# Kernel tuning notes

Measured on AMD Instinct MI355X. Metric: run time of the kernel, lower is better.

## Reference

```python
import jax, jax.numpy as jnp
import numpy as np

B, M, D, DH, DV = 16384, 3, 2048, 1024, 512

def setup_inputs() -> dict:
    key = jax.random.key(0)
    kx, kq, kk, kv, kf = jax.random.split(key, 5)
    x = jax.random.normal(kx, (B, M, D), dtype=jnp.float32)
    # nn.Linear weights are [out, in]; q/k/v scaled by 1/32 as in __init__
    Wq = jax.random.normal(kq, (DH, D), dtype=jnp.float32) / 32.0
    Wk = jax.random.normal(kk, (DH, D), dtype=jnp.float32) / 32.0
    Wv = jax.random.normal(kv, (DV, D), dtype=jnp.float32) / 32.0
    Wfc = jax.random.normal(kf, (1, DV), dtype=jnp.float32)
    return {"x": x, "Wq": Wq, "Wk": Wk, "Wv": Wv, "Wfc": Wfc}

def reference(x, Wq, Wk, Wv, Wfc):
    # q,k: [B,M,DH]; v: [B,M,DV]
    q = jnp.einsum('bmd,hd->bmh', x, Wq)
    k = jnp.einsum('bmd,hd->bmh', x, Wk)
    v = jnp.einsum('bmd,vd->bmv', x, Wv)
    qk = jnp.einsum('bih,bjh->bij', q, k)          # [B,M,M]
    attn = jax.nn.softmax(qk, axis=2)
    attn = jnp.sum(attn, axis=1) / M               # [B,M] (sum over queries, avg)
    z = jnp.einsum('bm,bmv->bv', attn, v)          # [B,DV]
    return z @ Wfc.T                               # [B,1]
```

## Files before the change

### kernel.cpp

```cpp
#include <hip/hip_runtime.h>
#include <hip/hip_bf16.h>
#include <stdint.h>
#include <stddef.h>

#define B_   16384
#define M_   3
#define D_   2048
#define DH_  1024
#define DV_  512
#define ROWS (B_ * M_)
#define NOUT (2 * DH_)

typedef _Float16 f16;
typedef f16   f16x8 __attribute__((ext_vector_type(8)));
typedef float f32x4 __attribute__((ext_vector_type(4)));

__device__ __forceinline__ void async16(const void* g, void* l) {
  __builtin_amdgcn_global_load_lds(
      (const __attribute__((address_space(1))) void*)g,
      (__attribute__((address_space(3))) void*)l, 16, 0, 0);
}

__global__ void k_wvf(const float* __restrict__ Wv, const float* __restrict__ Wfc,
                      float* __restrict__ wvf) {
  int dl = threadIdx.x & 31;
  int vs = threadIdx.x >> 5;
  int d = blockIdx.x * 32 + dl;
  float acc = 0.f;
  #pragma unroll 8
  for (int v = vs * 64; v < vs * 64 + 64; ++v)
    acc += Wfc[v] * Wv[(size_t)v * D_ + d];
  __shared__ float red[8][32];
  red[vs][dl] = acc;
  __syncthreads();
  if (threadIdx.x < 32) {
    float s = 0.f;
    #pragma unroll
    for (int i = 0; i < 8; ++i) s += red[i][threadIdx.x];
    wvf[blockIdx.x * 32 + threadIdx.x] = s;
  }
}

__global__ void k_castw(const float* __restrict__ Wq, const float* __restrict__ Wk,
                        f16* __restrict__ Wh) {
  int t = blockIdx.x * 256 + threadIdx.x;
  int idx = t * 8;
  int j = idx >> 11;
  int d = idx & (D_ - 1);
  const float* src = (j < DH_) ? (Wq + (size_t)j * D_ + d)
                               : (Wk + (size_t)(j - DH_) * D_ + d);
  f32x4 a = *(const f32x4*)src;
  f32x4 b = *(const f32x4*)(src + 4);
  f16x8 h;
  h[0] = (f16)a[0]; h[1] = (f16)a[1]; h[2] = (f16)a[2]; h[3] = (f16)a[3];
  h[4] = (f16)b[0]; h[5] = (f16)b[1]; h[6] = (f16)b[2]; h[7] = (f16)b[3];
  *(f16x8*)(Wh + (size_t)idx) = h;
}

__global__ void k_prep(const float* __restrict__ x, const float* __restrict__ wvf,
                       f16* __restrict__ Xh, float* __restrict__ vf) {
  int w = threadIdx.x >> 6, lane = threadIdx.x & 63;
  int row = blockIdx.x * 4 + w;
  const float* xr = x + (size_t)row * D_;
  f16* xo = Xh + (size_t)row * D_;
  float acc = 0.f;
  #pragma unroll
  for (int p = 0; p < 4; ++p) {
    int col = p * 512 + lane * 8;
    f32x4 a = *(const f32x4*)(xr + col);
    f32x4 b = *(const f32x4*)(xr + col + 4);
    f32x4 wa = *(const f32x4*)(wvf + col);
    f32x4 wb = *(const f32x4*)(wvf + col + 4);
    f16x8 h;
    h[0] = (f16)a[0]; h[1] = (f16)a[1]; h[2] = (f16)a[2]; h[3] = (f16)a[3];
    h[4] = (f16)b[0]; h[5] = (f16)b[1]; h[6] = (f16)b[2]; h[7] = (f16)b[3];
    *(f16x8*)(xo + col) = h;
    acc += a[0]*wa[0] + a[1]*wa[1] + a[2]*wa[2] + a[3]*wa[3]
         + b[0]*wb[0] + b[1]*wb[1] + b[2]*wb[2] + b[3]*wb[3];
  }
  #pragma unroll
  for (int off = 1; off < 64; off <<= 1) acc += __shfl_xor(acc, off);
  if (lane == 0) vf[row] = acc;
}

__global__ __launch_bounds__(256, 3) void k_gemm(const f16* __restrict__ Xh,
                                                 const f16* __restrict__ Wh,
                                                 f16* __restrict__ QK) {
  const int ct = blockIdx.x;
  const int rt = blockIdx.y;
  const int tid = threadIdx.x;
  const int w = tid >> 6, lane = tid & 63;
  const int wr = w >> 1, wc = w & 1;

  __shared__ __align__(16) f16 lds_a[128 * 64];
  __shared__ __align__(16) f16 lds_b[128 * 64];

  f32x4 acc[4][4] = {};

  const int srow = lane >> 3;
  const int schunk = (lane & 7) ^ srow;
  const int scol = schunk * 8;

  const f16* gA[4]; const f16* gB[4];
  f16 *la[4], *lb[4];
  #pragma unroll
  for (int t = 0; t < 4; ++t) {
    int rowA = w * 32 + t * 8;
    gA[t] = Xh + (size_t)(rt * 128 + rowA + srow) * D_ + scol;
    gB[t] = Wh + (size_t)(ct * 128 + rowA + srow) * D_ + scol;
    la[t] = &lds_a[rowA * 64];
    lb[t] = &lds_b[rowA * 64];
  }

  const int m = lane & 15;
  const int kq = lane >> 4;
  const f16* fa0 = &lds_a[(size_t)(wr * 64 + m) * 64 + ((kq    ) ^ (m & 7)) * 8];
  const f16* fa1 = &lds_a[(size_t)(wr * 64 + m) * 64 + ((kq + 4) ^ (m & 7)) * 8];
  const f16* fb0 = &lds_b[(size_t)(wc * 64 + m) * 64 + ((kq    ) ^ (m & 7)) * 8];
  const f16* fb1 = &lds_b[(size_t)(wc * 64 + m) * 64 + ((kq + 4) ^ (m & 7)) * 8];

  for (int k0 = 0; k0 < D_; k0 += 64) {
    #pragma unroll
    for (int t = 0; t < 4; ++t) async16(gA[t] + k0, la[t]);
    #pragma unroll
    for (int t = 0; t < 4; ++t) async16(gB[t] + k0, lb[t]);
    __syncthreads();
    {
      f16x8 af[4], bf[4];
      #pragma unroll
      for (int i = 0; i < 4; ++i) af[i] = *(const f16x8*)(fa0 + i * 16 * 64);
      #pragma unroll
      for (int j = 0; j < 4; ++j) bf[j] = *(const f16x8*)(fb0 + j * 16 * 64);
      #pragma unroll
      for (int i = 0; i < 4; ++i)
        #pragma unroll
        for (int j = 0; j < 4; ++j)
          acc[i][j] = __builtin_amdgcn_mfma_f32_16x16x32_f16(af[i], bf[j], acc[i][j], 0, 0, 0);
    }
    {
      f16x8 af[4], bf[4];
      #pragma unroll
      for (int i = 0; i < 4; ++i) af[i] = *(const f16x8*)(fa1 + i * 16 * 64);
      #pragma unroll
      for (int j = 0; j < 4; ++j) bf[j] = *(const f16x8*)(fb1 + j * 16 * 64);
      #pragma unroll
      for (int i = 0; i < 4; ++i)
        #pragma unroll
        for (int j = 0; j < 4; ++j)
          acc[i][j] = __builtin_amdgcn_mfma_f32_16x16x32_f16(af[i], bf[j], acc[i][j], 0, 0, 0);
    }
    __syncthreads();
  }

  const int r0 = rt * 128 + wr * 64 + (lane >> 4) * 4;
  const int c0 = ct * 128 + wc * 64 + (lane & 15);
  #pragma unroll
  for (int i = 0; i < 4; ++i)
    #pragma unroll
    for (int j = 0; j < 4; ++j)
      #pragma unroll
      for (int r = 0; r < 4; ++r)
        QK[(size_t)(r0 + i * 16 + r) * NOUT + (c0 + j * 16)] = (f16)acc[i][j][r];
}

__global__ void k_attn(const f16* __restrict__ QK, const float* __restrict__ vf,
                       float* __restrict__ out) {
  int w = threadIdx.x >> 6, lane = threadIdx.x & 63;
  int b = blockIdx.x * 4 + w;
  const f16* base = QK + (size_t)b * M_ * NOUT;
  f16x8 q[3][2], k[3][2];
  #pragma unroll
  for (int i = 0; i < 3; ++i) {
    q[i][0] = *(const f16x8*)(base + i * NOUT + lane * 8);
    q[i][1] = *(const f16x8*)(base + i * NOUT + 512 + lane * 8);
    k[i][0] = *(const f16x8*)(base + i * NOUT + 1024 + lane * 8);
    k[i][1] = *(const f16x8*)(base + i * NOUT + 1536 + lane * 8);
  }
  float s[3][3];
  #pragma unroll
  for (int i = 0; i < 3; ++i)
    #pragma unroll
    for (int j = 0; j < 3; ++j) {
      float a = 0.f;
      #pragma unroll
      for (int c = 0; c < 2; ++c)
        #pragma unroll
        for (int t = 0; t < 8; ++t)
          a += (float)q[i][c][t] * (float)k[j][c][t];
      s[i][j] = a;
    }
  #pragma unroll
  for (int i = 0; i < 3; ++i)
    #pragma unroll
    for (int j = 0; j < 3; ++j)
      #pragma unroll
      for (int off = 1; off < 64; off <<= 1)
        s[i][j] += __shfl_xor(s[i][j], off);
  if (lane == 0) {
    float attn[3] = {0.f, 0.f, 0.f};
    #pragma unroll
    for (int i = 0; i < 3; ++i) {
      float m = fmaxf(s[i][0], fmaxf(s[i][1], s[i][2]));
      float e0 = expf(s[i][0] - m), e1 = expf(s[i][1] - m), e2 = expf(s[i][2] - m);
      float inv = 1.f / (e0 + e1 + e2);
      attn[0] += e0 * inv; attn[1] += e1 * inv; attn[2] += e2 * inv;
    }
    float o = attn[0] * vf[b * 3 + 0] + attn[1] * vf[b * 3 + 1] + attn[2] * vf[b * 3 + 2];
    out[b] = o * (1.f / 3.f);
  }
}

extern "C" void kernel_launch(void* const* d_in, const int* in_sizes, int n_in,
                              void* d_out, int out_size, void* d_ws, size_t ws_size,
                              hipStream_t stream) {
  const float* x   = (const float*)d_in[0];
  const float* Wq  = (const float*)d_in[1];
  const float* Wk  = (const float*)d_in[2];
  const float* Wv  = (const float*)d_in[3];
  const float* Wfc = (const float*)d_in[4];
  float* out = (float*)d_out;

  char* ws = (char*)d_ws;
  f16*   Xh  = (f16*)(ws);
  f16*   QK  = (f16*)(ws + 201326592ull);
  f16*   Wh  = (f16*)(ws + 402653184ull);
  float* wvf = (float*)(ws + 411041792ull);
  float* vf  = (float*)(ws + 411049984ull);

  k_wvf  <<<64,             256, 0, stream>>>(Wv, Wfc, wvf);
  k_castw<<<2048,           256, 0, stream>>>(Wq, Wk, Wh);
  k_prep <<<ROWS / 4,       256, 0, stream>>>(x, wvf, Xh, vf);
  k_gemm <<<dim3(16, 384),  256, 0, stream>>>(Xh, Wh, QK);
  k_attn <<<B_ / 4,         256, 0, stream>>>(QK, vf, out);
}
```

Before: 1.011 ms.

## Fuse QK dot products into GEMM epilogue with per-head-tile partial scores

The GEMM's column tiles now pair 64 Q columns with the matching 64 K columns, and row tiles are aligned to 42 whole batches of 126 rows. Each block stages its Q and K tile in LDS and computes partial 3x3 scores over its 64-head slice, writing 144 floats per batch instead of the full fp16 QK matrix. A small final kernel sums the partials and applies softmax. This removes the large QK write and read-back at the cost of roughly 2% wasted rows in the padded tiles and a serial LDS epilogue.

New measurement: 976.8 us. 1.03x faster.

```diff
diff --git a/kernel.cpp b/kernel.cpp
--- a/kernel.cpp
+++ b/kernel.cpp
@@ -9,7 +9,10 @@
 #define DH_  1024
 #define DV_  512
 #define ROWS (B_ * M_)
-#define NOUT (2 * DH_)
+#define RT_ROWS 126
+#define RT_BATCH 42
+#define NRT 391
+#define NHT 16
 
 typedef _Float16 f16;
 typedef f16   f16x8 __attribute__((ext_vector_type(8)));
@@ -85,8 +88,8 @@
 
 __global__ __launch_bounds__(256, 3) void k_gemm(const f16* __restrict__ Xh,
                                                  const f16* __restrict__ Wh,
-                                                 f16* __restrict__ QK) {
-  const int ct = blockIdx.x;
+                                                 float* __restrict__ S_part) {
+  const int ht = blockIdx.x;
   const int rt = blockIdx.y;
   const int tid = threadIdx.x;
   const int w = tid >> 6, lane = tid & 63;
@@ -105,11 +108,15 @@
   f16 *la[4], *lb[4];
   #pragma unroll
   for (int t = 0; t < 4; ++t) {
-    int rowA = w * 32 + t * 8;
-    gA[t] = Xh + (size_t)(rt * 128 + rowA + srow) * D_ + scol;
-    gB[t] = Wh + (size_t)(ct * 128 + rowA + srow) * D_ + scol;
-    la[t] = &lds_a[rowA * 64];
-    lb[t] = &lds_b[rowA * 64];
+    int rowT = w * 32 + t * 8;
+    int ra = rt * RT_ROWS + rowT + srow;
+    if (ra > ROWS - 1) ra = ROWS - 1;
+    gA[t] = Xh + (size_t)ra * D_ + scol;
+    int c = rowT + srow;
+    int rb = (c < 64) ? (ht * 64 + c) : (DH_ + ht * 64 + (c - 64));
+    gB[t] = Wh + (size_t)rb * D_ + scol;
+    la[t] = &lds_a[rowT * 64];
+    lb[t] = &lds_b[rowT * 64];
   }
 
   const int m = lane & 15;
@@ -152,62 +159,58 @@
     __syncthreads();
   }
 
-  const int r0 = rt * 128 + wr * 64 + (lane >> 4) * 4;
-  const int c0 = ct * 128 + wc * 64 + (lane & 15);
-  #pragma unroll
-  for (int i = 0; i < 4; ++i)
-    #pragma unroll
-    for (int j = 0; j < 4; ++j)
-      #pragma unroll
-      for (int r = 0; r < 4; ++r)
-        QK[(size_t)(r0 + i * 16 + r) * NOUT + (c0 + j * 16)] = (f16)acc[i][j][r];
-}
-
-__global__ void k_attn(const f16* __restrict__ QK, const float* __restrict__ vf,
-                       float* __restrict__ out) {
-  int w = threadIdx.x >> 6, lane = threadIdx.x & 63;
-  int b = blockIdx.x * 4 + w;
-  const f16* base = QK + (size_t)b * M_ * NOUT;
-  f16x8 q[3][2], k[3][2];
+  {
+    f16* dst = wc ? lds_b : lds_a;
+    const int rbase = wr * 64 + (lane >> 4) * 4;
+    const int hcol = lane & 15;
+    #pragma unroll
+    for (int i = 0; i < 4; ++i)
+      #pragma unroll
+      for (int j = 0; j < 4; ++j)
+        #pragma unroll
+        for (int r = 0; r < 4; ++r)
+          dst[(size_t)(rbase + i * 16 + r) * 64 + j * 16 + hcol] = (f16)acc[i][j][r];
+  }
+  __syncthreads();
+
+  for (int p = tid; p < RT_BATCH * 9; p += 256) {
+    int bl = p / 9;
+    int ij = p - bl * 9;
+    int i = ij / 3, j = ij - i * 3;
+    const f16* qp = &lds_a[(size_t)(bl * 3 + i) * 64];
+    const f16* kp = &lds_b[(size_t)(bl * 3 + j) * 64];
+    float s = 0.f;
+    #pragma unroll
+    for (int hc = 0; hc < 8; ++hc) {
+      f16x8 qa = *(const f16x8*)(qp + hc * 8);
+      f16x8 ka = *(const f16x8*)(kp + hc * 8);
+      #pragma unroll
+      for (int t = 0; t < 8; ++t) s += (float)qa[t] * (float)ka[t];
+    }
+    int b = rt * RT_BATCH + bl;
+    if (b < B_) S_part[(size_t)b * (NHT * 9) + ht * 9 + ij] = s;
+  }
+}
+
+__global__ void k_final(const float* __restrict__ S_part, const float* __restrict__ vf,
+                        float* __restrict__ out) {
+  int b = blockIdx.x * 256 + threadIdx.x;
+  const float* sp = S_part + (size_t)b * (NHT * 9);
+  float s[9] = {0,0,0,0,0,0,0,0,0};
+  #pragma unroll
+  for (int ht = 0; ht < NHT; ++ht)
+    #pragma unroll
+    for (int ij = 0; ij < 9; ++ij) s[ij] += sp[ht * 9 + ij];
+  float attn[3] = {0.f, 0.f, 0.f};
   #pragma unroll
   for (int i = 0; i < 3; ++i) {
-    q[i][0] = *(const f16x8*)(base + i * NOUT + lane * 8);
-    q[i][1] = *(const f16x8*)(base + i * NOUT + 512 + lane * 8);
-    k[i][0] = *(const f16x8*)(base + i * NOUT + 1024 + lane * 8);
-    k[i][1] = *(const f16x8*)(base + i * NOUT + 1536 + lane * 8);
-  }
-  float s[3][3];
-  #pragma unroll
-  for (int i = 0; i < 3; ++i)
-    #pragma unroll
-    for (int j = 0; j < 3; ++j) {
-      float a = 0.f;
-      #pragma unroll
-      for (int c = 0; c < 2; ++c)
-        #pragma unroll
-        for (int t = 0; t < 8; ++t)
-          a += (float)q[i][c][t] * (float)k[j][c][t];
-      s[i][j] = a;
-    }
-  #pragma unroll
-  for (int i = 0; i < 3; ++i)
-    #pragma unroll
-    for (int j = 0; j < 3; ++j)
-      #pragma unroll
-      for (int off = 1; off < 64; off <<= 1)
-        s[i][j] += __shfl_xor(s[i][j], off);
-  if (lane == 0) {
-    float attn[3] = {0.f, 0.f, 0.f};
-    #pragma unroll
-    for (int i = 0; i < 3; ++i) {
-      float m = fmaxf(s[i][0], fmaxf(s[i][1], s[i][2]));
-      float e0 = expf(s[i][0] - m), e1 = expf(s[i][1] - m), e2 = expf(s[i][2] - m);
-      float inv = 1.f / (e0 + e1 + e2);
-      attn[0] += e0 * inv; attn[1] += e1 * inv; attn[2] += e2 * inv;
-    }
-    float o = attn[0] * vf[b * 3 + 0] + attn[1] * vf[b * 3 + 1] + attn[2] * vf[b * 3 + 2];
-    out[b] = o * (1.f / 3.f);
-  }
+    float m = fmaxf(s[i*3+0], fmaxf(s[i*3+1], s[i*3+2]));
+    float e0 = __expf(s[i*3+0] - m), e1 = __expf(s[i*3+1] - m), e2 = __expf(s[i*3+2] - m);
+    float inv = 1.f / (e0 + e1 + e2);
+    attn[0] += e0 * inv; attn[1] += e1 * inv; attn[2] += e2 * inv;
+  }
+  float o = attn[0] * vf[b * 3 + 0] + attn[1] * vf[b * 3 + 1] + attn[2] * vf[b * 3 + 2];
+  out[b] = o * (1.f / 3.f);
 }
 
 extern "C" void kernel_launch(void* const* d_in, const int* in_sizes, int n_in,
@@ -221,15 +224,15 @@
   float* out = (float*)d_out;
 
   char* ws = (char*)d_ws;
-  f16*   Xh  = (f16*)(ws);
-  f16*   QK  = (f16*)(ws + 201326592ull);
-  f16*   Wh  = (f16*)(ws + 402653184ull);
-  float* wvf = (float*)(ws + 411041792ull);
-  float* vf  = (float*)(ws + 411049984ull);
-
-  k_wvf  <<<64,             256, 0, stream>>>(Wv, Wfc, wvf);
-  k_castw<<<2048,           256, 0, stream>>>(Wq, Wk, Wh);
-  k_prep <<<ROWS / 4,       256, 0, stream>>>(x, wvf, Xh, vf);
-  k_gemm <<<dim3(16, 384),  256, 0, stream>>>(Xh, Wh, QK);
-  k_attn <<<B_ / 4,         256, 0, stream>>>(QK, vf, out);
-}
+  f16*   Xh     = (f16*)(ws);
+  f16*   Wh     = (f16*)(ws + 201326592ull);
+  float* wvf    = (float*)(ws + 209715200ull);
+  float* vf     = (float*)(ws + 209723392ull);
+  float* S_part = (float*)(ws + 209920000ull);
+
+  k_wvf  <<<64,              256, 0, stream>>>(Wv, Wfc, wvf);
+  k_castw<<<2048,            256, 0, stream>>>(Wq, Wk, Wh);
+  k_prep <<<ROWS / 4,        256, 0, stream>>>(x, wvf, Xh, vf);
+  k_gemm <<<dim3(NHT, NRT),  256, 0, stream>>>(Xh, Wh, S_part);
+  k_final<<<B_ / 256,        256, 0, stream>>>(S_part, vf, out);
+}
```
